# Kernel optimization log

Measured on AMD Instinct MI355X. Metric: run time of the kernel, lower is better.

## Reference

```python
import jax, jax.numpy as jnp
import numpy as np
from jax import lax

B, T, D, A = 32, 2048, 1024, 1024

def setup_inputs() -> dict:
    key = jax.random.key(0)
    ks = jax.random.split(key, 8)
    s = 1.0 / np.sqrt(D)
    return {
        "query": jax.random.normal(ks[0], (B, 1, D), jnp.float32),
        "value": jax.random.normal(ks[1], (B, T, D), jnp.float32),
        "last_attn": jax.random.uniform(ks[2], (B, T), jnp.float32),
        "conv_w": jax.random.normal(ks[3], (A, 1, 3), jnp.float32) * 0.1,
        "conv_b": jnp.zeros((A,), jnp.float32),
        "Wq": jax.random.normal(ks[4], (A, D), jnp.float32) * s,
        "Wv": jax.random.normal(ks[5], (A, D), jnp.float32) * s,
        "bias": jax.random.uniform(ks[6], (A,), jnp.float32, -0.1, 0.1),
        "fc_w": jax.random.normal(ks[7], (1, A), jnp.float32) * (1.0 / np.sqrt(A)),
        "fc_b": jnp.zeros((1,), jnp.float32),
    }

def reference(query, value, last_attn, conv_w, conv_b, Wq, Wv, bias, fc_w, fc_b):
    # location conv1d: (B,1,T) -> (B,A,T), kernel 3, pad 1
    loc = lax.conv_general_dilated(
        last_attn[:, None, :], conv_w, window_strides=(1,), padding="SAME",
        dimension_numbers=("NCH", "OIH", "NCH"))
    loc = loc + conv_b[None, :, None]
    loc = jnp.transpose(loc, (0, 2, 1))  # (B, T, A)
    # fused add + bias + tanh; query proj (B,1,A) broadcasts over T
    hidden = jnp.tanh(query @ Wq.T + value @ Wv.T + loc + bias)  # (B, T, A)
    energy = (hidden @ fc_w.T + fc_b)[..., 0]  # (B, T)
    attn = jax.nn.softmax(energy, axis=-1)  # (B, T)
    context = jnp.einsum("bt,btd->bd", attn, value)[:, None, :]  # (B, 1, D)
    return context, attn
```

## Files before the change

kernel.cpp:

```cpp
#include <hip/hip_runtime.h>
#include <stdint.h>

#define AS1 __attribute__((address_space(1)))
#define AS3 __attribute__((address_space(3)))

typedef __bf16 bf16x8 __attribute__((ext_vector_type(8)));
typedef float  f32x4  __attribute__((ext_vector_type(4)));

__global__ __launch_bounds__(256) void cast_bf16(const float* __restrict__ in,
                                                 __bf16* __restrict__ out, int n8) {
    int i = blockIdx.x * 256 + threadIdx.x;
    if (i >= n8) return;
    const float4* p = (const float4*)in + (size_t)i * 2;
    float4 x = p[0], y = p[1];
    bf16x8 v;
    v[0] = (__bf16)x.x; v[1] = (__bf16)x.y; v[2] = (__bf16)x.z; v[3] = (__bf16)x.w;
    v[4] = (__bf16)y.x; v[5] = (__bf16)y.y; v[6] = (__bf16)y.z; v[7] = (__bf16)y.w;
    *((bf16x8*)out + i) = v;
}

__global__ __launch_bounds__(256) void prep_qb2(const float* __restrict__ q,
                                                const float* __restrict__ Wq,
                                                const float* __restrict__ bias,
                                                const float* __restrict__ convb,
                                                float* __restrict__ qb2) {
    int wid  = threadIdx.x >> 6;
    int lane = threadIdx.x & 63;
    int a    = blockIdx.x * 4 + wid;
    const float* wr_ = Wq + (size_t)a * 1024;
    float w[16];
#pragma unroll
    for (int j = 0; j < 16; ++j) w[j] = wr_[lane + 64 * j];
    float bb = bias[a] + convb[a];
    for (int b = 0; b < 32; ++b) {
        const float* qr = q + (size_t)b * 1024;
        float s = 0.f;
#pragma unroll
        for (int j = 0; j < 16; ++j) s += w[j] * qr[lane + 64 * j];
        for (int m = 1; m < 64; m <<= 1) s += __shfl_xor(s, m);
        if (lane == 0) qb2[b * 1024 + a] = s + bb;
    }
}

__global__ __launch_bounds__(512, 2) void gemm_fused(
    const __bf16* __restrict__ Abf,
    const __bf16* __restrict__ Bbf,
    const float*  __restrict__ qb2,
    const float*  __restrict__ la,
    const float*  __restrict__ convw,
    const float*  __restrict__ fcw,
    float* __restrict__ ep)
{
    constexpr int K = 1024, NT = 16;
    __shared__ __bf16 As[2][256 * 64];
    __shared__ __bf16 Bs[2][256 * 64];

    const int tid  = threadIdx.x;
    const int lane = tid & 63;
    const int wid  = tid >> 6;
    const int wr   = wid >> 2, wc = wid & 3;

    const int bid = blockIdx.x;
    const int swz = (bid & 7) * 128 + (bid >> 3);
    const int rt  = swz >> 2;
    const int ct  = swz & 3;
    const int rowBase = rt * 256;
    const int colBase = ct * 256;

    f32x4 acc[8][4] = {};

    auto STAGE = [&](int buf, int k0) {
#pragma unroll
        for (int is = 0; is < 4; ++is) {
            int idx16 = is * 512 + tid;
            int r     = idx16 >> 3;
            int ssw   = (idx16 ^ r) & 7;
            const __bf16* ga = Abf + (size_t)(rowBase + r) * K + k0 + ssw * 8;
            __builtin_amdgcn_global_load_lds((AS1 void*)ga, (AS3 void*)(&As[buf][idx16 * 8]), 16, 0, 0);
            const __bf16* gb = Bbf + (size_t)(colBase + r) * K + k0 + ssw * 8;
            __builtin_amdgcn_global_load_lds((AS1 void*)gb, (AS3 void*)(&Bs[buf][idx16 * 8]), 16, 0, 0);
        }
    };

    auto COMPUTE = [&](int buf) {
        bf16x8 bfr[4][2];
#pragma unroll
        for (int ni = 0; ni < 4; ++ni)
#pragma unroll
            for (int kk = 0; kk < 2; ++kk) {
                int row  = wc * 64 + ni * 16 + (lane & 15);
                int slot = (kk * 4 + (lane >> 4)) ^ (row & 7);
                bfr[ni][kk] = *(const bf16x8*)(&Bs[buf][row * 64 + slot * 8]);
            }
#pragma unroll
        for (int mh = 0; mh < 2; ++mh)
#pragma unroll
            for (int kk = 0; kk < 2; ++kk) {
                bf16x8 af[4];
#pragma unroll
                for (int i = 0; i < 4; ++i) {
                    int row  = wr * 128 + (mh * 4 + i) * 16 + (lane & 15);
                    int slot = (kk * 4 + (lane >> 4)) ^ (row & 7);
                    af[i] = *(const bf16x8*)(&As[buf][row * 64 + slot * 8]);
                }
                __builtin_amdgcn_s_setprio(1);
#pragma unroll
                for (int i = 0; i < 4; ++i)
#pragma unroll
                    for (int ni = 0; ni < 4; ++ni)
                        acc[mh * 4 + i][ni] = __builtin_amdgcn_mfma_f32_16x16x32_bf16(
                            af[i], bfr[ni][kk], acc[mh * 4 + i][ni], 0, 0, 0);
                __builtin_amdgcn_s_setprio(0);
            }
    };

    STAGE(0, 0);
    __syncthreads();
#pragma unroll 1
    for (int t = 0; t < NT; ++t) {
        if (t + 1 < NT) STAGE((t + 1) & 1, (t + 1) * 64);
        COMPUTE(t & 1);
        __syncthreads();
    }

    const int b     = rowBase >> 11;
    const int tTile = rowBase & 2047;
    const float* lab  = la  + (size_t)b * 2048;
    const float* qrow = qb2 + (size_t)b * 1024;

    float cw0[4], cw1[4], cw2[4], fv[4], qv[4];
#pragma unroll
    for (int ni = 0; ni < 4; ++ni) {
        int a = colBase + wc * 64 + ni * 16 + (lane & 15);
        cw0[ni] = convw[a * 3 + 0];
        cw1[ni] = convw[a * 3 + 1];
        cw2[ni] = convw[a * 3 + 2];
        fv[ni]  = fcw[a];
        qv[ni]  = qrow[a];
    }
    float* eps = (float*)&As[0][0];
    const int g4 = (lane >> 4) * 4;
#pragma unroll
    for (int mi = 0; mi < 8; ++mi) {
#pragma unroll
        for (int j = 0; j < 4; ++j) {
            int rloc = wr * 128 + mi * 16 + g4 + j;
            int t = tTile + rloc;
            float p1 = lab[t];
            float p0 = (t > 0)    ? lab[t - 1] : 0.f;
            float p2 = (t < 2047) ? lab[t + 1] : 0.f;
            float sum = 0.f;
#pragma unroll
            for (int ni = 0; ni < 4; ++ni) {
                float e = acc[mi][ni][j] + qv[ni] + cw0[ni] * p0 + cw1[ni] * p1 + cw2[ni] * p2;
                float h = 1.f - 2.f / (1.f + __expf(2.f * e));
                sum += fv[ni] * h;
            }
            sum += __shfl_xor(sum, 1);
            sum += __shfl_xor(sum, 2);
            sum += __shfl_xor(sum, 4);
            sum += __shfl_xor(sum, 8);
            if ((lane & 15) == 0) eps[rloc * 4 + wc] = sum;
        }
    }
    __syncthreads();
    if (tid < 256) {
        float e = eps[tid * 4 + 0] + eps[tid * 4 + 1] + eps[tid * 4 + 2] + eps[tid * 4 + 3];
        ep[(size_t)ct * 65536 + rowBase + tid] = e;
    }
}

__global__ __launch_bounds__(256) void softmax_rows(const float* __restrict__ ep,
                                                    float* __restrict__ attn) {
    int b = blockIdx.x, tid = threadIdx.x;
    float* o = attn + (size_t)b * 2048;
    __shared__ float red[4], red2[4];

    float e8[8];
#pragma unroll
    for (int k = 0; k < 8; ++k) {
        int t = tid + 256 * k;
        float s = 0.f;
#pragma unroll
        for (int ct = 0; ct < 4; ++ct) s += ep[(size_t)ct * 65536 + b * 2048 + t];
        e8[k] = s;
    }

    float m = -1e30f;
#pragma unroll
    for (int k = 0; k < 8; ++k) m = fmaxf(m, e8[k]);
    for (int s = 1; s < 64; s <<= 1) m = fmaxf(m, __shfl_xor(m, s));
    if ((tid & 63) == 0) red[tid >> 6] = m;
    __syncthreads();
    m = fmaxf(fmaxf(red[0], red[1]), fmaxf(red[2], red[3]));

    float s = 0.f, vals[8];
#pragma unroll
    for (int k = 0; k < 8; ++k) { vals[k] = __expf(e8[k] - m); s += vals[k]; }
    for (int t = 1; t < 64; t <<= 1) s += __shfl_xor(s, t);
    if ((tid & 63) == 0) red2[tid >> 6] = s;
    __syncthreads();
    s = red2[0] + red2[1] + red2[2] + red2[3];
    float inv = 1.f / s;
#pragma unroll
    for (int k = 0; k < 8; ++k) o[tid + 256 * k] = vals[k] * inv;
}

__global__ __launch_bounds__(256) void context_kernel(const float* __restrict__ attn,
                                                      const __bf16* __restrict__ vbf,
                                                      float* __restrict__ ctx) {
    int b = blockIdx.x, tc = blockIdx.y, tid = threadIdx.x;
    int half = tid >> 7, dc = tid & 127;
    const float*  ab = attn + (size_t)b * 2048 + tc * 256 + half * 128;
    const __bf16* vb = vbf + ((size_t)(b * 2048 + tc * 256 + half * 128)) * 1024 + dc * 8;
    float c[8] = {};
#pragma unroll 4
    for (int t = 0; t < 128; ++t) {
        float  w = ab[t];
        bf16x8 v = *(const bf16x8*)(vb + (size_t)t * 1024);
#pragma unroll
        for (int k = 0; k < 8; ++k) c[k] += w * (float)v[k];
    }
    float* out = ctx + (size_t)b * 1024 + dc * 8;
#pragma unroll
    for (int k = 0; k < 8; ++k) atomicAdd(out + k, c[k]);
}

extern "C" void kernel_launch(void* const* d_in, const int* in_sizes, int n_in,
                              void* d_out, int out_size, void* d_ws, size_t ws_size,
                              hipStream_t stream) {
    const float* query     = (const float*)d_in[0];
    const float* value     = (const float*)d_in[1];
    const float* last_attn = (const float*)d_in[2];
    const float* conv_w    = (const float*)d_in[3];
    const float* conv_b    = (const float*)d_in[4];
    const float* Wq        = (const float*)d_in[5];
    const float* Wv        = (const float*)d_in[6];
    const float* bias      = (const float*)d_in[7];
    const float* fc_w      = (const float*)d_in[8];

    float* ctx  = (float*)d_out;
    float* attn = (float*)d_out + 32 * 1024;

    const size_t VBF_B  = (size_t)65536 * 1024 * 2;
    const size_t WVBF_B = (size_t)1024 * 1024 * 2;
    const size_t QB2_B  = (size_t)32 * 1024 * 4;
    const size_t EP_B   = (size_t)4 * 32 * 2048 * 4;
    if (ws_size < VBF_B + WVBF_B + QB2_B + EP_B) return;

    char*   ws   = (char*)d_ws;
    __bf16* vbf  = (__bf16*)ws;
    __bf16* wvbf = (__bf16*)(ws + VBF_B);
    float*  qb2  = (float*)(ws + VBF_B + WVBF_B);
    float*  ep   = (float*)(ws + VBF_B + WVBF_B + QB2_B);

    hipMemsetAsync(ctx, 0, 32 * 1024 * sizeof(float), stream);

    cast_bf16<<<512, 256, 0, stream>>>(Wv, wvbf, 1024 * 1024 / 8);
    prep_qb2<<<256, 256, 0, stream>>>(query, Wq, bias, conv_b, qb2);
    cast_bf16<<<32768, 256, 0, stream>>>(value, vbf, 65536 * 1024 / 8);

    gemm_fused<<<1024, 512, 0, stream>>>(vbf, wvbf, qb2, last_attn, conv_w, fc_w, ep);

    softmax_rows<<<32, 256, 0, stream>>>(ep, attn);
    dim3 gc(32, 8);
    context_kernel<<<gc, 256, 0, stream>>>(attn, vbf, ctx);
}
```

Baseline: 343.0 us.

## Interleave split global-to-LDS staging with MFMA phases using explicit barriers

The GEMM main loop now splits each K-tile's A and B staging into halves and issues them inside four compute phases. Each phase reads LDS fragments, issues its share of loads, then waits on barriers before running its MFMAs. Explicit vmcnt/lgkmcnt waits and sched_barriers replace __syncthreads, so global loads overlap more finely with matrix math. The cost is many more barriers per iteration, plus a hand-tuned vmcnt count whose correctness depends on load ordering.

```diff
diff --git a/kernel.cpp b/kernel.cpp
--- a/kernel.cpp
+++ b/kernel.cpp
@@ -69,59 +69,89 @@
 
     f32x4 acc[8][4] = {};
 
-    auto STAGE = [&](int buf, int k0) {
-#pragma unroll
-        for (int is = 0; is < 4; ++is) {
-            int idx16 = is * 512 + tid;
+    auto STAGE_A = [&](int buf, int half, int k0) {
+#pragma unroll
+        for (int is = 0; is < 2; ++is) {
+            int idx16 = half * 1024 + is * 512 + tid;
             int r     = idx16 >> 3;
             int ssw   = (idx16 ^ r) & 7;
-            const __bf16* ga = Abf + (size_t)(rowBase + r) * K + k0 + ssw * 8;
-            __builtin_amdgcn_global_load_lds((AS1 void*)ga, (AS3 void*)(&As[buf][idx16 * 8]), 16, 0, 0);
-            const __bf16* gb = Bbf + (size_t)(colBase + r) * K + k0 + ssw * 8;
-            __builtin_amdgcn_global_load_lds((AS1 void*)gb, (AS3 void*)(&Bs[buf][idx16 * 8]), 16, 0, 0);
+            const __bf16* g = Abf + (size_t)(rowBase + r) * K + k0 + ssw * 8;
+            __builtin_amdgcn_global_load_lds((AS1 void*)g, (AS3 void*)(&As[buf][idx16 * 8]), 16, 0, 0);
         }
     };
-
-    auto COMPUTE = [&](int buf) {
+    auto STAGE_B = [&](int buf, int half, int k0) {
+#pragma unroll
+        for (int is = 0; is < 2; ++is) {
+            int idx16 = half * 1024 + is * 512 + tid;
+            int r     = idx16 >> 3;
+            int ssw   = (idx16 ^ r) & 7;
+            const __bf16* g = Bbf + (size_t)(colBase + r) * K + k0 + ssw * 8;
+            __builtin_amdgcn_global_load_lds((AS1 void*)g, (AS3 void*)(&Bs[buf][idx16 * 8]), 16, 0, 0);
+        }
+    };
+
+#define DO_PHASE(bufv, kk, mh, READB, STAGE_STMT)                              \
+    {                                                                          \
+        if (READB) {                                                           \
+            _Pragma("unroll")                                                  \
+            for (int ni = 0; ni < 4; ++ni) {                                   \
+                int row  = wc * 64 + ni * 16 + (lane & 15);                    \
+                int slot = ((kk) * 4 + (lane >> 4)) ^ (row & 7);               \
+                bfr[ni][kk] = *(const bf16x8*)(&Bs[bufv][row * 64 + slot * 8]);\
+            }                                                                  \
+        }                                                                      \
+        bf16x8 af[4];                                                          \
+        _Pragma("unroll")                                                      \
+        for (int i = 0; i < 4; ++i) {                                          \
+            int row  = wr * 128 + ((mh) * 4 + i) * 16 + (lane & 15);           \
+            int slot = ((kk) * 4 + (lane >> 4)) ^ (row & 7);                   \
+            af[i] = *(const bf16x8*)(&As[bufv][row * 64 + slot * 8]);          \
+        }                                                                      \
+        STAGE_STMT;                                                            \
+        __builtin_amdgcn_s_barrier();                                          \
+        asm volatile("s_waitcnt lgkmcnt(0)" ::: "memory");                     \
+        __builtin_amdgcn_sched_barrier(0);                                     \
+        __builtin_amdgcn_s_setprio(1);                                         \
+        _Pragma("unroll")                                                      \
+        for (int i = 0; i < 4; ++i)                                            \
+            _Pragma("unroll")                                                  \
+            for (int ni = 0; ni < 4; ++ni)                                     \
+                acc[(mh) * 4 + i][ni] = __builtin_amdgcn_mfma_f32_16x16x32_bf16(\
+                    af[i], bfr[ni][kk], acc[(mh) * 4 + i][ni], 0, 0, 0);       \
+        __builtin_amdgcn_s_setprio(0);                                         \
+        __builtin_amdgcn_s_barrier();                                          \
+    }
+
+    STAGE_A(0, 0, 0); STAGE_A(0, 1, 0);
+    STAGE_B(0, 0, 0); STAGE_B(0, 1, 0);
+
+#pragma unroll 1
+    for (int t = 0; t < NT - 1; ++t) {
+        const int buf = t & 1;
+        const int kn  = (t + 1) * 64;
+        __builtin_amdgcn_sched_barrier(0);
+        STAGE_A(buf ^ 1, 0, kn);
+        __builtin_amdgcn_sched_barrier(0);
+        asm volatile("s_waitcnt vmcnt(2)" ::: "memory");
+        __builtin_amdgcn_s_barrier();
+        __builtin_amdgcn_sched_barrier(0);
         bf16x8 bfr[4][2];
-#pragma unroll
-        for (int ni = 0; ni < 4; ++ni)
-#pragma unroll
-            for (int kk = 0; kk < 2; ++kk) {
-                int row  = wc * 64 + ni * 16 + (lane & 15);
-                int slot = (kk * 4 + (lane >> 4)) ^ (row & 7);
-                bfr[ni][kk] = *(const bf16x8*)(&Bs[buf][row * 64 + slot * 8]);
-            }
-#pragma unroll
-        for (int mh = 0; mh < 2; ++mh)
-#pragma unroll
-            for (int kk = 0; kk < 2; ++kk) {
-                bf16x8 af[4];
-#pragma unroll
-                for (int i = 0; i < 4; ++i) {
-                    int row  = wr * 128 + (mh * 4 + i) * 16 + (lane & 15);
-                    int slot = (kk * 4 + (lane >> 4)) ^ (row & 7);
-                    af[i] = *(const bf16x8*)(&As[buf][row * 64 + slot * 8]);
-                }
-                __builtin_amdgcn_s_setprio(1);
-#pragma unroll
-                for (int i = 0; i < 4; ++i)
-#pragma unroll
-                    for (int ni = 0; ni < 4; ++ni)
-                        acc[mh * 4 + i][ni] = __builtin_amdgcn_mfma_f32_16x16x32_bf16(
-                            af[i], bfr[ni][kk], acc[mh * 4 + i][ni], 0, 0, 0);
-                __builtin_amdgcn_s_setprio(0);
-            }
-    };
-
-    STAGE(0, 0);
-    __syncthreads();
-#pragma unroll 1
-    for (int t = 0; t < NT; ++t) {
-        if (t + 1 < NT) STAGE((t + 1) & 1, (t + 1) * 64);
-        COMPUTE(t & 1);
-        __syncthreads();
-    }
+        DO_PHASE(buf, 0, 0, true,  STAGE_A(buf ^ 1, 1, kn));
+        DO_PHASE(buf, 0, 1, false, STAGE_B(buf ^ 1, 0, kn));
+        DO_PHASE(buf, 1, 0, true,  STAGE_B(buf ^ 1, 1, kn));
+        DO_PHASE(buf, 1, 1, false, (void)0);
+    }
+    {
+        asm volatile("s_waitcnt vmcnt(0)" ::: "memory");
+        __builtin_amdgcn_s_barrier();
+        __builtin_amdgcn_sched_barrier(0);
+        bf16x8 bfr[4][2];
+        DO_PHASE(1, 0, 0, true,  (void)0);
+        DO_PHASE(1, 0, 1, false, (void)0);
+        DO_PHASE(1, 1, 0, true,  (void)0);
+        DO_PHASE(1, 1, 1, false, (void)0);
+    }
+#undef DO_PHASE
 
     const int b     = rowBase >> 11;
     const int tTile = rowBase & 2047;
```

Measured after the change: 335.6 us. 1.02x faster.
